# Kernel optimization log

Hardware: AMD Instinct MI355X
Metric: run time of the kernel (lower is better)

The kernel has to match this reference:

```python
import jax, jax.numpy as jnp
import numpy as np

B, S, F_IN = 8, 4096, 256      # batch, frames, mel bins
C = 256                        # model_complexity (out_features of attention)
G = 8                          # n_heads (groups)
K = 31                         # w_size (local window, odd)
F_OUT = 88                     # output_features (piano keys)
PAD = (K - 1) // 2


def setup_inputs() -> dict:
    key = jax.random.key(0)
    ks = jax.random.split(key, 7)
    s = 0.05
    return {
        "spec": jax.random.normal(ks[0], (B, S, F_IN), jnp.float32),
        "W_q": jax.random.normal(ks[1], (F_IN, C), jnp.float32) * s,
        "W_k": jax.random.normal(ks[2], (F_IN, C), jnp.float32) * s,
        "W_v": jax.random.normal(ks[3], (F_IN, C), jnp.float32) * s,
        "rel": jax.random.normal(ks[4], (C, K), jnp.float32),
        "W_lin": jax.random.normal(ks[5], (C, F_OUT), jnp.float32) * s,
        "b_lin": jax.random.normal(ks[6], (F_OUT,), jnp.float32) * s,
    }


def reference(spec, W_q, W_k, W_v, rel, W_lin, b_lin):
    b, s, _ = spec.shape
    d = C // G  # per-head dim
    # QKV projections (no bias, as in the module)
    q = spec @ W_q                                             # [B,S,C]
    padded = jnp.pad(spec, ((0, 0), (PAD, PAD), (0, 0)))       # [B,S+2p,F]
    k = padded @ W_k                                           # [B,S+2p,C]
    v = padded @ W_v
    # unfold: window index [S,K]
    idx = jnp.arange(s)[:, None] + jnp.arange(K)[None, :]      # [S,K]
    kw = jnp.transpose(k[:, idx, :], (0, 1, 3, 2))             # [B,S,C,K]
    vw = jnp.transpose(v[:, idx, :], (0, 1, 3, 2))             # [B,S,C,K]
    kw = kw + rel                                              # positional bias [C,K]
    kw = kw.reshape(b, s, G, d, K)
    vw = vw.reshape(b, s, G, d, K)
    qh = q.reshape(b, s, G, d)
    energy = jnp.einsum('bsgd,bsgdk->bsgk', qh, kw)            # [B,S,G,K]
    attn = jax.nn.softmax(energy, axis=-1)                     # [B,S,G,K]
    out = jnp.einsum('bsgk,bsgdk->bsgd', attn, vw).reshape(b, s, C)
    frame_pred = jax.nn.sigmoid(out @ W_lin + b_lin)           # [B,S,F_OUT]
    return frame_pred, attn
```

## Files before the change

### kernel.cpp

```cpp
#include <hip/hip_runtime.h>
#include <hip/hip_bf16.h>
#include <math.h>

#define B_   8
#define S_   4096
#define FIN  256
#define C_   256
#define G_   8
#define D_   32
#define K_   31
#define PAD_ 15
#define FOUT 88

typedef __bf16 bf16;
typedef __attribute__((ext_vector_type(8))) __bf16 bf16x8;
typedef __attribute__((ext_vector_type(4))) __bf16 bf16x4;
typedef __attribute__((ext_vector_type(4))) float f32x4;

#define MFMA16(A, B, C) __builtin_amdgcn_mfma_f32_16x16x32_bf16(A, B, C, 0, 0, 0)

__global__ __launch_bounds__(256) void prep_all(
    const float* __restrict__ Wq, const float* __restrict__ Wk,
    const float* __restrict__ Wv, const float* __restrict__ Wl,
    const float* __restrict__ rel,
    bf16* __restrict__ bth, bf16* __restrict__ btl,
    bf16* __restrict__ wlh, bf16* __restrict__ wll,
    bf16* __restrict__ Vt,
    bf16* __restrict__ relH, bf16* __restrict__ relL)
{
    const int bid = blockIdx.x;
    const int t   = threadIdx.x;

    if (bid < 768) {
        const int w = bid >> 8;
        const int k = bid & 255;
        const float* W = (w == 0) ? Wq : (w == 1) ? Wk : Wv;
        const float x = W[(size_t)k * 256 + t];
        const bf16 h = (bf16)x;
        const size_t o = (size_t)w * 65536 + (size_t)t * 256 + k;
        bth[o] = h;
        btl[o] = (bf16)(x - (float)h);
    } else if (bid < 896) {
        const int k = (bid - 768) * 2 + (t >> 7);
        const int n = t & 127;
        const float x = (n < FOUT) ? Wl[(size_t)k * FOUT + n] : 0.f;
        const bf16 h = (bf16)x;
        wlh[(size_t)n * 256 + k] = h;
        wll[(size_t)n * 256 + k] = (bf16)(x - (float)h);
    } else if (bid < 1024) {
        const int idx = (bid - 896) * 256 + t;
        const int bd  = idx >> 4;
        const int pos = (idx & 15) * 4;
        const int off = (pos < 16) ? pos : 4096 + pos;
        bf16x4 z = {};
        *(bf16x4*)&Vt[(size_t)bd * 4160 + off] = z;
    } else {
        const int idx = (bid - 1024) * 256 + t;
        const int g = idx >> 10, k = (idx >> 5) & 31, d = idx & 31;
        const float v = (k < 31) ? rel[(size_t)(g * 32 + d) * 31 + k] : 0.f;
        const bf16 h = (bf16)v;
        relH[idx] = h;
        relL[idx] = (bf16)(v - (float)h);
    }
}

__device__ __forceinline__ void gload16(const bf16* g, bf16* l) {
    __builtin_amdgcn_global_load_lds(
        (const __attribute__((address_space(1))) void*)g,
        (__attribute__((address_space(3))) void*)l, 16, 0, 0);
}

__device__ __forceinline__ void gload16f(const float* g, float* l) {
    __builtin_amdgcn_global_load_lds(
        (const __attribute__((address_space(1))) void*)g,
        (__attribute__((address_space(3))) void*)l, 16, 0, 0);
}

__device__ __forceinline__ void stage_tile(const bf16* g, bf16* l, int t) {
    const int lg = ((t & 3) ^ ((t >> 3) & 3)) * 8;
    const int r0 = t >> 2;
    const int r1 = 64 + (t >> 2);
    const int u0 = (t & ~63) * 8;
    gload16(g + (size_t)r0 * 256 + lg, l + u0);
    gload16(g + (size_t)r1 * 256 + lg, l + u0 + 2048);
}

__device__ __forceinline__ bf16x8 frag_ld(const bf16* l, int r, int cl) {
    return *(const bf16x8*)&l[r * 32 + ((cl ^ ((r >> 1) & 3)) << 3)];
}

__device__ __forceinline__ void stage_tileA(const float* g, float* l, int t) {
#pragma unroll
    for (int i = 0; i < 4; ++i) {
        const int li  = i * 256 + t;
        const int row = li >> 3;
        const int sc  = li & 7;
        const int src = row * 256 + ((sc ^ (row & 7)) << 2);
        gload16f(g + src, l + ((i << 8) + (t & ~63)) * 4);
    }
}

__device__ __forceinline__ void frag_ldA(const float* A, int r, int cl,
                                         bf16x8* hi, bf16x8* lo) {
    const int base = r * 32;
    const f32x4 a0 = *(const f32x4*)&A[base + ((( 2 * cl)     ^ (r & 7)) << 2)];
    const f32x4 a1 = *(const f32x4*)&A[base + (((2 * cl + 1)  ^ (r & 7)) << 2)];
    bf16x8 h, l;
#pragma unroll
    for (int j = 0; j < 4; ++j) {
        const bf16 h0 = (bf16)a0[j]; h[j]     = h0; l[j]     = (bf16)(a0[j] - (float)h0);
        const bf16 h1 = (bf16)a1[j]; h[4 + j] = h1; l[4 + j] = (bf16)(a1[j] - (float)h1);
    }
    *hi = h; *lo = l;
}

__device__ __forceinline__ bf16x8 frag_ldA_hi(const float* A, int r, int cl) {
    const int base = r * 32;
    const f32x4 a0 = *(const f32x4*)&A[base + ((( 2 * cl)     ^ (r & 7)) << 2)];
    const f32x4 a1 = *(const f32x4*)&A[base + (((2 * cl + 1)  ^ (r & 7)) << 2)];
    bf16x8 h;
#pragma unroll
    for (int j = 0; j < 4; ++j) { h[j] = (bf16)a0[j]; h[4 + j] = (bf16)a1[j]; }
    return h;
}

__global__ __launch_bounds__(256) void qkv_mfma(
    const float* __restrict__ spec,
    const bf16* __restrict__ bth, const bf16* __restrict__ btl,
    bf16* __restrict__ Qh, bf16* __restrict__ Ql,
    bf16* __restrict__ Kh, bf16* __restrict__ Kl,
    bf16* __restrict__ Vt)
{
    __shared__ char ldsq[32768];
    float* Af = (float*)ldsq;
    bf16*  Bh = (bf16*)(ldsq + 16384);
    bf16*  Bl = (bf16*)(ldsq + 24576);

    const int t   = threadIdx.x;
    const int swz = ((blockIdx.x & 7) * 192) + (blockIdx.x >> 3);
    const int mt  = swz / 6, nt = swz % 6;
    const int wt  = nt >> 1;
    const int m0  = mt * 128, n0 = (nt & 1) * 128;
    const bool three = (wt < 2);

    const float* a_g = spec + (size_t)m0 * 256;
    const bf16* bh_g = bth + (size_t)wt * 65536 + (size_t)n0 * 256;
    const bf16* bl_g = btl + (size_t)wt * 65536 + (size_t)n0 * 256;

    const int lane = t & 63, wid = t >> 6;
    const int wr = (wid >> 1) * 64, wc = (wid & 1) * 64;
    const int fr = lane & 15, cl = lane >> 4;

    f32x4 acc[4][4];
#pragma unroll
    for (int m = 0; m < 4; ++m)
#pragma unroll
        for (int n = 0; n < 4; ++n)
            acc[m][n] = (f32x4){0.f, 0.f, 0.f, 0.f};

    for (int ks = 0; ks < 8; ++ks) {
        const int ko = ks * 32;
        stage_tileA(a_g + ko, Af, t);
        stage_tile(bh_g + ko, Bh, t);
        stage_tile(bl_g + ko, Bl, t);
        __syncthreads();

        bf16x8 bh8[4], bl8[4];
#pragma unroll
        for (int n = 0; n < 4; ++n) {
            bh8[n] = frag_ld(Bh, wc + n * 16 + fr, cl);
            bl8[n] = frag_ld(Bl, wc + n * 16 + fr, cl);
        }
        if (three) {
            bf16x8 ahh[4], ahl[4];
#pragma unroll
            for (int m = 0; m < 4; ++m)
                frag_ldA(Af, wr + m * 16 + fr, cl, &ahh[m], &ahl[m]);
#pragma unroll
            for (int m = 0; m < 4; ++m)
#pragma unroll
                for (int n = 0; n < 4; ++n) {
                    acc[m][n] = MFMA16(ahh[m], bh8[n], acc[m][n]);
                    acc[m][n] = MFMA16(ahh[m], bl8[n], acc[m][n]);
                    acc[m][n] = MFMA16(ahl[m], bh8[n], acc[m][n]);
                }
        } else {
            bf16x8 ahh[4];
#pragma unroll
            for (int m = 0; m < 4; ++m)
                ahh[m] = frag_ldA_hi(Af, wr + m * 16 + fr, cl);
#pragma unroll
            for (int m = 0; m < 4; ++m)
#pragma unroll
                for (int n = 0; n < 4; ++n) {
                    acc[m][n] = MFMA16(ahh[m], bh8[n], acc[m][n]);
                    acc[m][n] = MFMA16(ahh[m], bl8[n], acc[m][n]);
                }
        }
        __syncthreads();
    }

    if (wt < 2) {
        bf16* Oh = (wt == 0) ? Qh : Kh;
        bf16* Ol = (wt == 0) ? Ql : Kl;
#pragma unroll
        for (int m = 0; m < 4; ++m) {
            const int gr = m0 + wr + m * 16 + cl * 4;
#pragma unroll
            for (int n = 0; n < 4; ++n) {
                const int gc = n0 + wc + n * 16 + fr;
#pragma unroll
                for (int i = 0; i < 4; ++i) {
                    const float v = acc[m][n][i];
                    const bf16 hh = (bf16)v;
                    const size_t off = (size_t)(gr + i) * 256 + gc;
                    Oh[off] = hh;
                    Ol[off] = (bf16)(v - (float)hh);
                }
            }
        }
    } else {
#pragma unroll
        for (int m = 0; m < 4; ++m) {
            const int gr = m0 + wr + m * 16 + cl * 4;
            const int bb = gr >> 12, sr = gr & 4095;
#pragma unroll
            for (int n = 0; n < 4; ++n) {
                const int gc = n0 + wc + n * 16 + fr;
                bf16x4 pk;
#pragma unroll
                for (int i = 0; i < 4; ++i) pk[i] = (bf16)acc[m][n][i];
                *(bf16x4*)&Vt[(size_t)(bb * 256 + gc) * 4160 + 16 + sr] = pk;
            }
        }
    }
}

__global__ __launch_bounds__(256) void attn_mfma(
    const bf16* __restrict__ Qh, const bf16* __restrict__ Ql,
    const bf16* __restrict__ Kh, const bf16* __restrict__ Kl,
    const bf16* __restrict__ Vt,
    const bf16* __restrict__ relH, const bf16* __restrict__ relL,
    float* __restrict__ attn, bf16* __restrict__ Obf)
{
    __shared__ char ldsb[18432];

    const int t    = threadIdx.x;
    const int wid  = t >> 6;
    const int lane = t & 63;
    const int fr   = lane & 15;
    const int q    = lane >> 4;
    const int f7   = fr & 7;
    const int sl   = lane >> 2;
    const int jj   = lane & 3;

    const int bid2 = ((blockIdx.x & 7) << 8) | (blockIdx.x >> 3);
    const int sg0  = bid2 << 4;
    const int b    = sg0 >> 12;
    const int s0   = sg0 & 4095;

    float* Rbuf = (float*)(ldsb + wid * 4608);
    float* Pf32 = Rbuf;
    bf16*  Pbuf = (bf16*) (ldsb + wid * 4608 + 2304);

    {
        uint* p32 = (uint*)Pbuf;
#pragma unroll
        for (int j = 0; j < 9; ++j) p32[lane + 64 * j] = 0u;
    }

    const size_t rowQ = (size_t)(sg0 + fr) * 256;

#pragma unroll
    for (int h = 0; h < 2; ++h) {
        asm volatile("" ::: "memory");
        const int g   = wid * 2 + h;
        const int dof = g * 32 + q * 8;

        const bf16x8 qh8 = *(const bf16x8*)&Qh[rowQ + dof];
        const bf16x8 ql8 = *(const bf16x8*)&Ql[rowQ + dof];

        f32x4 e0, e1, e2;
#pragma unroll
        for (int tau = 0; tau < 3; ++tau) {
            const int trel = s0 - 16 + tau * 16 + fr;
            bf16x8 kh8 = {}, kl8 = {};
            if ((unsigned)trel < 4096u) {
                const size_t rk = ((size_t)(b << 12) + trel) * 256 + dof;
                kh8 = *(const bf16x8*)&Kh[rk];
                kl8 = *(const bf16x8*)&Kl[rk];
            }
            f32x4 a = (f32x4){0.f, 0.f, 0.f, 0.f};
            a = MFMA16(kh8, qh8, a);
            a = MFMA16(kh8, ql8, a);
            a = MFMA16(kl8, qh8, a);
            if (tau == 0) e0 = a; else if (tau == 1) e1 = a; else e2 = a;
        }

#pragma unroll
        for (int kap = 0; kap < 2; ++kap) {
            const size_t ro = (size_t)(g * 32 + kap * 16 + fr) * 32 + q * 8;
            const bf16x8 rh8 = *(const bf16x8*)&relH[ro];
            const bf16x8 rl8 = *(const bf16x8*)&relL[ro];
            f32x4 rc = (f32x4){0.f, 0.f, 0.f, 0.f};
            rc = MFMA16(rh8, qh8, rc);
            rc = MFMA16(rh8, ql8, rc);
            rc = MFMA16(rl8, qh8, rc);
#pragma unroll
            for (int r = 0; r < 4; ++r)
                Rbuf[(kap * 16 + q * 4 + r) * 18 + fr] = rc[r];
        }

        float ev[3][4];
        float mx = -3.0e38f;
#pragma unroll
        for (int tau = 0; tau < 3; ++tau) {
#pragma unroll
            for (int r = 0; r < 4; ++r) {
                const int rp = q * 4 + r;
                const int kk = tau * 16 + rp - fr - 1;
                const float eb = (tau == 0) ? e0[r] : (tau == 1) ? e1[r] : e2[r];
                float v = eb + Rbuf[(kk & 31) * 18 + fr];
                const bool valid = (tau == 1) || ((tau == 0) ? (rp > fr) : (rp < fr));
                v = valid ? v : -3.0e38f;
                ev[tau][r] = v;
                mx = fmaxf(mx, v);
            }
        }
        mx = fmaxf(mx, __shfl_xor(mx, 16));
        mx = fmaxf(mx, __shfl_xor(mx, 32));
        float sum = 0.f;
#pragma unroll
        for (int tau = 0; tau < 3; ++tau)
#pragma unroll
            for (int r = 0; r < 4; ++r) {
                const float p = __expf(ev[tau][r] - mx);
                ev[tau][r] = p;
                sum += p;
            }
        sum += __shfl_xor(sum, 16);
        sum += __shfl_xor(sum, 32);
        const float inv = 1.f / sum;

#pragma unroll
        for (int tau = 0; tau < 3; ++tau)
#pragma unroll
            for (int r = 0; r < 4; ++r) {
                const int rp = q * 4 + r;
                const int kk = tau * 16 + rp - fr - 1;
                const bool valid = (tau == 1) || ((tau == 0) ? (rp > fr) : (rp < fr));
                if (valid) {
                    const float p = ev[tau][r] * inv;
                    Pf32[fr * 36 + kk] = p;
                    const int tl = tau * 16 + rp;
                    Pbuf[fr * 72 + (((tl >> 3) ^ f7) << 3) + (tl & 7)] = (bf16)p;
                }
            }

        asm volatile("" ::: "memory");
        {
            float* arow = &attn[((size_t)(sg0 + sl) * 8 + g) * 31];
#pragma unroll
            for (int i = 0; i < 8; ++i) {
                const int k = jj + 4 * i;
                if (k < 31) arow[k] = Pf32[sl * 36 + k];
            }
        }

        asm volatile("" ::: "memory");
        const bf16x8 a0 = *(const bf16x8*)&Pbuf[fr * 72 + ((q ^ f7) << 3)];
        const bf16x8 a1 = *(const bf16x8*)&Pbuf[fr * 72 + (((4 + q) ^ f7) << 3)];
#pragma unroll
        for (int dl = 0; dl < 2; ++dl) {
            const size_t vrow = (size_t)(b * 256 + g * 32 + dl * 16 + fr) * 4160
                              + s0 + q * 8;
            const bf16x8 v0 = *(const bf16x8*)&Vt[vrow];
            const bf16x8 v1 = *(const bf16x8*)&Vt[vrow + 32];
            f32x4 o = (f32x4){0.f, 0.f, 0.f, 0.f};
            o = MFMA16(v0, a0, o);
            o = MFMA16(v1, a1, o);
            bf16x4 pk;
#pragma unroll
            for (int r = 0; r < 4; ++r) pk[r] = (bf16)o[r];
            *(bf16x4*)&Obf[(size_t)(sg0 + fr) * 256 + g * 32 + dl * 16 + (q << 2)] = pk;
        }
    }
}

__global__ __launch_bounds__(256) void frame_mfma(
    const bf16* __restrict__ O,
    const bf16* __restrict__ wlh, const bf16* __restrict__ wll,
    const float* __restrict__ bl, float* __restrict__ frame)
{
    __shared__ bf16 lds[3 * 4096];

    const int t  = threadIdx.x;
    const int m0 = blockIdx.x * 128;

    const bf16* a_g = O + (size_t)m0 * 256;

    const int lane = t & 63, wid = t >> 6;
    const int wr = (wid >> 1) * 64, wc = (wid & 1) * 64;
    const int fr = lane & 15, cl = lane >> 4;

    f32x4 acc[4][4];
#pragma unroll
    for (int m = 0; m < 4; ++m)
#pragma unroll
        for (int n = 0; n < 4; ++n)
            acc[m][n] = (f32x4){0.f, 0.f, 0.f, 0.f};

    for (int ks = 0; ks < 8; ++ks) {
        const int ko = ks * 32;
        stage_tile(a_g + ko, lds, t);
        stage_tile(wlh + ko, lds + 4096, t);
        stage_tile(wll + ko, lds + 8192, t);
        __syncthreads();

        bf16x8 ah[4], bh[4], bl4[4];
#pragma unroll
        for (int m = 0; m < 4; ++m) ah[m] = frag_ld(lds, wr + m * 16 + fr, cl);
#pragma unroll
        for (int n = 0; n < 4; ++n) {
            bh[n]  = frag_ld(lds + 4096, wc + n * 16 + fr, cl);
            bl4[n] = frag_ld(lds + 8192, wc + n * 16 + fr, cl);
        }
#pragma unroll
        for (int m = 0; m < 4; ++m)
#pragma unroll
            for (int n = 0; n < 4; ++n) {
                acc[m][n] = MFMA16(ah[m], bh[n],  acc[m][n]);
                acc[m][n] = MFMA16(ah[m], bl4[n], acc[m][n]);
            }
        __syncthreads();
    }

#pragma unroll
    for (int m = 0; m < 4; ++m) {
        const int gr = m0 + wr + m * 16 + cl * 4;
#pragma unroll
        for (int n = 0; n < 4; ++n) {
            const int gc = wc + n * 16 + fr;
            if (gc < FOUT) {
                const float bb = bl[gc];
#pragma unroll
                for (int i = 0; i < 4; ++i) {
                    const float x = acc[m][n][i] + bb;
                    frame[(size_t)(gr + i) * FOUT + gc] = 1.f / (1.f + __expf(-x));
                }
            }
        }
    }
}

extern "C" void kernel_launch(void* const* d_in, const int* in_sizes, int n_in,
                              void* d_out, int out_size, void* d_ws, size_t ws_size,
                              hipStream_t stream) {
    (void)in_sizes; (void)n_in; (void)out_size; (void)ws_size;
    const float* spec = (const float*)d_in[0];
    const float* Wq   = (const float*)d_in[1];
    const float* Wk   = (const float*)d_in[2];
    const float* Wv   = (const float*)d_in[3];
    const float* rel  = (const float*)d_in[4];
    const float* Wl   = (const float*)d_in[5];
    const float* bl   = (const float*)d_in[6];

    float* frame = (float*)d_out;
    float* attn  = frame + (size_t)B_ * S_ * FOUT;

    bf16* bth  = (bf16*)((char*)d_out + 33554432);
    bf16* btl  = bth + 3 * 65536;
    bf16* relH = (bf16*)d_out;
    bf16* relL = relH + 8192;

    bf16* Qh  = (bf16*)d_ws;
    bf16* Ql  = Qh + (size_t)8388608;
    bf16* Kh  = Ql + (size_t)8388608;
    bf16* Kl  = Kh + (size_t)8388608;
    bf16* Vt  = Kl + (size_t)8388608;
    bf16* wlh = Vt + (size_t)8 * 256 * 4160;
    bf16* wll = wlh + 128 * 256;

    prep_all  <<<dim3(1056), 256, 0, stream>>>(Wq, Wk, Wv, Wl, rel,
                                               bth, btl, wlh, wll, Vt, relH, relL);
    qkv_mfma  <<<dim3(1536), 256, 0, stream>>>(spec, bth, btl, Qh, Ql, Kh, Kl, Vt);
    attn_mfma <<<dim3(2048), 256, 0, stream>>>(Qh, Ql, Kh, Kl, Vt, relH, relL, attn, Qh);
    frame_mfma<<<dim3(256),  256, 0, stream>>>(Qh, wlh, wll, bl, frame);
}
```

Baseline: 116.7 us.

## Load GEMM fragments directly from global memory instead of staging through LDS

The QKV projection and frame-output GEMM kernels no longer stage A and B tiles into shared memory with global_load_lds and barriers. Each lane now loads its MFMA fragments straight from global memory (via L2/L1), and the K loop is fully unrolled. This removes LDS traffic and __syncthreads stalls, and lets the compiler hoist loads across iterations. In exchange, data shared between waves is fetched redundantly from cache, and the uncoalesced 16-byte row-strided loads may raise memory latency and register pressure.

Measured after the change: 169.1 us. 44.8% more time.

```diff
diff --git a/kernel.cpp b/kernel.cpp
--- a/kernel.cpp
+++ b/kernel.cpp
@@ -64,66 +64,6 @@
     }
 }
 
-__device__ __forceinline__ void gload16(const bf16* g, bf16* l) {
-    __builtin_amdgcn_global_load_lds(
-        (const __attribute__((address_space(1))) void*)g,
-        (__attribute__((address_space(3))) void*)l, 16, 0, 0);
-}
-
-__device__ __forceinline__ void gload16f(const float* g, float* l) {
-    __builtin_amdgcn_global_load_lds(
-        (const __attribute__((address_space(1))) void*)g,
-        (__attribute__((address_space(3))) void*)l, 16, 0, 0);
-}
-
-__device__ __forceinline__ void stage_tile(const bf16* g, bf16* l, int t) {
-    const int lg = ((t & 3) ^ ((t >> 3) & 3)) * 8;
-    const int r0 = t >> 2;
-    const int r1 = 64 + (t >> 2);
-    const int u0 = (t & ~63) * 8;
-    gload16(g + (size_t)r0 * 256 + lg, l + u0);
-    gload16(g + (size_t)r1 * 256 + lg, l + u0 + 2048);
-}
-
-__device__ __forceinline__ bf16x8 frag_ld(const bf16* l, int r, int cl) {
-    return *(const bf16x8*)&l[r * 32 + ((cl ^ ((r >> 1) & 3)) << 3)];
-}
-
-__device__ __forceinline__ void stage_tileA(const float* g, float* l, int t) {
-#pragma unroll
-    for (int i = 0; i < 4; ++i) {
-        const int li  = i * 256 + t;
-        const int row = li >> 3;
-        const int sc  = li & 7;
-        const int src = row * 256 + ((sc ^ (row & 7)) << 2);
-        gload16f(g + src, l + ((i << 8) + (t & ~63)) * 4);
-    }
-}
-
-__device__ __forceinline__ void frag_ldA(const float* A, int r, int cl,
-                                         bf16x8* hi, bf16x8* lo) {
-    const int base = r * 32;
-    const f32x4 a0 = *(const f32x4*)&A[base + ((( 2 * cl)     ^ (r & 7)) << 2)];
-    const f32x4 a1 = *(const f32x4*)&A[base + (((2 * cl + 1)  ^ (r & 7)) << 2)];
-    bf16x8 h, l;
-#pragma unroll
-    for (int j = 0; j < 4; ++j) {
-        const bf16 h0 = (bf16)a0[j]; h[j]     = h0; l[j]     = (bf16)(a0[j] - (float)h0);
-        const bf16 h1 = (bf16)a1[j]; h[4 + j] = h1; l[4 + j] = (bf16)(a1[j] - (float)h1);
-    }
-    *hi = h; *lo = l;
-}
-
-__device__ __forceinline__ bf16x8 frag_ldA_hi(const float* A, int r, int cl) {
-    const int base = r * 32;
-    const f32x4 a0 = *(const f32x4*)&A[base + ((( 2 * cl)     ^ (r & 7)) << 2)];
-    const f32x4 a1 = *(const f32x4*)&A[base + (((2 * cl + 1)  ^ (r & 7)) << 2)];
-    bf16x8 h;
-#pragma unroll
-    for (int j = 0; j < 4; ++j) { h[j] = (bf16)a0[j]; h[4 + j] = (bf16)a1[j]; }
-    return h;
-}
-
 __global__ __launch_bounds__(256) void qkv_mfma(
     const float* __restrict__ spec,
     const bf16* __restrict__ bth, const bf16* __restrict__ btl,
@@ -131,11 +71,6 @@
     bf16* __restrict__ Kh, bf16* __restrict__ Kl,
     bf16* __restrict__ Vt)
 {
-    __shared__ char ldsq[32768];
-    float* Af = (float*)ldsq;
-    bf16*  Bh = (bf16*)(ldsq + 16384);
-    bf16*  Bl = (bf16*)(ldsq + 24576);
-
     const int t   = threadIdx.x;
     const int swz = ((blockIdx.x & 7) * 192) + (blockIdx.x >> 3);
     const int mt  = swz / 6, nt = swz % 6;
@@ -143,14 +78,23 @@
     const int m0  = mt * 128, n0 = (nt & 1) * 128;
     const bool three = (wt < 2);
 
-    const float* a_g = spec + (size_t)m0 * 256;
-    const bf16* bh_g = bth + (size_t)wt * 65536 + (size_t)n0 * 256;
-    const bf16* bl_g = btl + (size_t)wt * 65536 + (size_t)n0 * 256;
-
     const int lane = t & 63, wid = t >> 6;
     const int wr = (wid >> 1) * 64, wc = (wid & 1) * 64;
     const int fr = lane & 15, cl = lane >> 4;
 
+    const float* aB[4];
+    const bf16*  hB[4];
+    const bf16*  lB[4];
+#pragma unroll
+    for (int m = 0; m < 4; ++m)
+        aB[m] = spec + (size_t)(m0 + wr + m * 16 + fr) * 256 + cl * 8;
+#pragma unroll
+    for (int n = 0; n < 4; ++n) {
+        const size_t bo = (size_t)wt * 65536 + (size_t)(n0 + wc + n * 16 + fr) * 256 + cl * 8;
+        hB[n] = bth + bo;
+        lB[n] = btl + bo;
+    }
+
     f32x4 acc[4][4];
 #pragma unroll
     for (int m = 0; m < 4; ++m)
@@ -158,46 +102,43 @@
         for (int n = 0; n < 4; ++n)
             acc[m][n] = (f32x4){0.f, 0.f, 0.f, 0.f};
 
+#pragma unroll
     for (int ks = 0; ks < 8; ++ks) {
         const int ko = ks * 32;
-        stage_tileA(a_g + ko, Af, t);
-        stage_tile(bh_g + ko, Bh, t);
-        stage_tile(bl_g + ko, Bl, t);
-        __syncthreads();
-
+
+        f32x4 af0[4], af1[4];
         bf16x8 bh8[4], bl8[4];
 #pragma unroll
+        for (int m = 0; m < 4; ++m) {
+            af0[m] = *(const f32x4*)(aB[m] + ko);
+            af1[m] = *(const f32x4*)(aB[m] + ko + 4);
+        }
+#pragma unroll
         for (int n = 0; n < 4; ++n) {
-            bh8[n] = frag_ld(Bh, wc + n * 16 + fr, cl);
-            bl8[n] = frag_ld(Bl, wc + n * 16 + fr, cl);
-        }
-        if (three) {
-            bf16x8 ahh[4], ahl[4];
-#pragma unroll
-            for (int m = 0; m < 4; ++m)
-                frag_ldA(Af, wr + m * 16 + fr, cl, &ahh[m], &ahl[m]);
-#pragma unroll
-            for (int m = 0; m < 4; ++m)
-#pragma unroll
-                for (int n = 0; n < 4; ++n) {
-                    acc[m][n] = MFMA16(ahh[m], bh8[n], acc[m][n]);
-                    acc[m][n] = MFMA16(ahh[m], bl8[n], acc[m][n]);
-                    acc[m][n] = MFMA16(ahl[m], bh8[n], acc[m][n]);
+            bh8[n] = *(const bf16x8*)(hB[n] + ko);
+            bl8[n] = *(const bf16x8*)(lB[n] + ko);
+        }
+
+#pragma unroll
+        for (int m = 0; m < 4; ++m) {
+            bf16x8 ahh, ahl;
+#pragma unroll
+            for (int j = 0; j < 4; ++j) {
+                const float x0 = af0[m][j], x1 = af1[m][j];
+                const bf16 h0 = (bf16)x0, h1 = (bf16)x1;
+                ahh[j] = h0; ahh[4 + j] = h1;
+                if (three) {
+                    ahl[j]     = (bf16)(x0 - (float)h0);
+                    ahl[4 + j] = (bf16)(x1 - (float)h1);
                 }
-        } else {
-            bf16x8 ahh[4];
-#pragma unroll
-            for (int m = 0; m < 4; ++m)
-                ahh[m] = frag_ldA_hi(Af, wr + m * 16 + fr, cl);
-#pragma unroll
-            for (int m = 0; m < 4; ++m)
-#pragma unroll
-                for (int n = 0; n < 4; ++n) {
-                    acc[m][n] = MFMA16(ahh[m], bh8[n], acc[m][n]);
-                    acc[m][n] = MFMA16(ahh[m], bl8[n], acc[m][n]);
-                }
-        }
-        __syncthreads();
+            }
+#pragma unroll
+            for (int n = 0; n < 4; ++n) {
+                acc[m][n] = MFMA16(ahh, bh8[n], acc[m][n]);
+                acc[m][n] = MFMA16(ahh, bl8[n], acc[m][n]);
+                if (three) acc[m][n] = MFMA16(ahl, bh8[n], acc[m][n]);
+            }
+        }
     }
 
     if (wt < 2) {
@@ -392,17 +333,26 @@
     const bf16* __restrict__ wlh, const bf16* __restrict__ wll,
     const float* __restrict__ bl, float* __restrict__ frame)
 {
-    __shared__ bf16 lds[3 * 4096];
-
     const int t  = threadIdx.x;
     const int m0 = blockIdx.x * 128;
-
-    const bf16* a_g = O + (size_t)m0 * 256;
 
     const int lane = t & 63, wid = t >> 6;
     const int wr = (wid >> 1) * 64, wc = (wid & 1) * 64;
     const int fr = lane & 15, cl = lane >> 4;
 
+    const bf16* aB[4];
+    const bf16* hB[4];
+    const bf16* lB[4];
+#pragma unroll
+    for (int m = 0; m < 4; ++m)
+        aB[m] = O + (size_t)(m0 + wr + m * 16 + fr) * 256 + cl * 8;
+#pragma unroll
+    for (int n = 0; n < 4; ++n) {
+        const size_t bo = (size_t)(wc + n * 16 + fr) * 256 + cl * 8;
+        hB[n] = wlh + bo;
+        lB[n] = wll + bo;
+    }
+
     f32x4 acc[4][4];
 #pragma unroll
     for (int m = 0; m < 4; ++m)
@@ -410,29 +360,24 @@
         for (int n = 0; n < 4; ++n)
             acc[m][n] = (f32x4){0.f, 0.f, 0.f, 0.f};
 
+#pragma unroll
     for (int ks = 0; ks < 8; ++ks) {
         const int ko = ks * 32;
-        stage_tile(a_g + ko, lds, t);
-        stage_tile(wlh + ko, lds + 4096, t);
-        stage_tile(wll + ko, lds + 8192, t);
-        __syncthreads();
-
-        bf16x8 ah[4], bh[4], bl4[4];
-#pragma unroll
-        for (int m = 0; m < 4; ++m) ah[m] = frag_ld(lds, wr + m * 16 + fr, cl);
+        bf16x8 ah[4], bh8[4], bl8[4];
+#pragma unroll
+        for (int m = 0; m < 4; ++m) ah[m] = *(const bf16x8*)(aB[m] + ko);
 #pragma unroll
         for (int n = 0; n < 4; ++n) {
-            bh[n]  = frag_ld(lds + 4096, wc + n * 16 + fr, cl);
-            bl4[n] = frag_ld(lds + 8192, wc + n * 16 + fr, cl);
+            bh8[n] = *(const bf16x8*)(hB[n] + ko);
+            bl8[n] = *(const bf16x8*)(lB[n] + ko);
         }
 #pragma unroll
         for (int m = 0; m < 4; ++m)
 #pragma unroll
             for (int n = 0; n < 4; ++n) {
-                acc[m][n] = MFMA16(ah[m], bh[n],  acc[m][n]);
-                acc[m][n] = MFMA16(ah[m], bl4[n], acc[m][n]);
-            }
-        __syncthreads();
+                acc[m][n] = MFMA16(ah[m], bh8[n], acc[m][n]);
+                acc[m][n] = MFMA16(ah[m], bl8[n], acc[m][n]);
+            }
     }
 
 #pragma unroll
```
